# Kernel optimization log

Measured on AMD Instinct MI355X. Metric: run time of the kernel, lower is better.

The kernel has to match this reference:

```python
import jax, jax.numpy as jnp
import numpy as np

N_NODES = 50000
N_EDGES = 800000
IN_CH = 16
OUT_CH = 16


def setup_inputs() -> dict:
    key = jax.random.key(0)
    ks = jax.random.split(key, 12)
    s = lambda d: 1.0 / np.sqrt(d)
    return {
        "x": jax.random.normal(ks[0], (N_NODES, IN_CH), jnp.float32),
        "edge_index": jax.random.randint(ks[1], (2, N_EDGES), 0, N_NODES, jnp.int64),
        "edge_attr": jax.random.uniform(ks[2], (N_EDGES, 8), jnp.float32),
        "W1": jax.random.normal(ks[3], (8, 100), jnp.float32) * s(8),
        "b1": jnp.zeros((100,), jnp.float32),
        "W2": jax.random.normal(ks[4], (100, 100), jnp.float32) * s(100),
        "b2": jnp.zeros((100,), jnp.float32),
        "W3": jax.random.normal(ks[5], (100, 100), jnp.float32) * s(100),
        "b3": jnp.zeros((100,), jnp.float32),
        "W4": jax.random.normal(ks[6], (100, IN_CH * OUT_CH), jnp.float32) * s(100),
        "b4": jnp.zeros((IN_CH * OUT_CH,), jnp.float32),
        "root": jax.random.normal(ks[7], (IN_CH, OUT_CH), jnp.float32) * s(IN_CH),
        "bias": jnp.zeros((OUT_CH,), jnp.float32),
    }


def reference(x, edge_index, edge_attr, W1, b1, W2, b2, W3, b3, W4, b4, root, bias):
    src, dst = edge_index[0], edge_index[1]
    # edge MLP -> per-edge weight matrix [E, in, out]
    h = jax.nn.relu(edge_attr @ W1 + b1)
    h = jax.nn.relu(h @ W2 + b2)
    h = jax.nn.relu(h @ W3 + b3)
    w = (h @ W4 + b4).reshape(-1, IN_CH, OUT_CH)
    # gather source features, per-edge matmul
    msg = jnp.einsum('ei,eio->eo', x[src], w)  # [E, out]
    # scatter-mean into destination nodes
    agg = jax.ops.segment_sum(msg, dst, num_segments=N_NODES)
    cnt = jax.ops.segment_sum(jnp.ones((msg.shape[0],), msg.dtype), dst, num_segments=N_NODES)
    agg = agg / jnp.maximum(cnt, 1.0)[:, None]
    return x @ root + agg + bias
```

## Files before the change

kernel.cpp:

```cpp
#include <hip/hip_runtime.h>
#include <hip/hip_bf16.h>

constexpr int N_NODES = 50000;
constexpr int E_TOTAL = 800000;
constexpr int EB   = 32;
constexpr int NT   = E_TOTAL / EB;
constexpr int GRID = 768;
constexpr int TPB  = 256;

typedef __attribute__((ext_vector_type(8)))  short bf16x8;
typedef __attribute__((ext_vector_type(16))) float f32x16;

constexpr size_t WS_CNT = 0;
constexpr size_t WS_W1  = 200704;
constexpr size_t WS_W2  = WS_W1 + 4096;
constexpr size_t WS_W3  = WS_W2 + 32768;
constexpr size_t WS_W4  = WS_W3 + 32768;

constexpr int L_HA  = 0;
constexpr int L_HB  = 8704;
constexpr int L_EA  = 17408;
constexpr int L_XS  = 18944;
constexpr int L_MSG = 21504;
constexpr int L_DST = 31744;
constexpr int L_TOT = 32000;

__device__ inline unsigned short bfb(float f) {
    __hip_bfloat16 h = __float2bfloat16(f);
    return __builtin_bit_cast(unsigned short, h);
}
__device__ inline unsigned pk2(float a, float b) {
    return (unsigned)bfb(a) | ((unsigned)bfb(b) << 16);
}
__device__ inline unsigned pk2r(float a, float b) {
    return pk2(fmaxf(a, 0.f), fmaxf(b, 0.f));
}

template<int IN_OFF, int OUT_OFF>
__device__ inline void layer32(char* sm, const bf16x8 (&wf)[8],
                               int wn, int l31, int g)
{
    const int e = l31;
    f32x16 acc = {};
#pragma unroll
    for (int ks = 0; ks < 8; ++ks) {
        const bf16x8 b = *reinterpret_cast<const bf16x8*>(sm + IN_OFF + e * 272 + ks * 32 + g * 16);
        acc = __builtin_amdgcn_mfma_f32_32x32x16_bf16(wf[ks], b, acc, 0, 0, 0);
    }
#pragma unroll
    for (int q = 0; q < 4; ++q) {
        uint2 pk;
        pk.x = pk2r(acc[4 * q + 0], acc[4 * q + 1]);
        pk.y = pk2r(acc[4 * q + 2], acc[4 * q + 3]);
        *reinterpret_cast<uint2*>(sm + OUT_OFF + e * 272 + 64 * wn + 16 * q + 8 * g) = pk;
    }
}

__global__ __launch_bounds__(TPB, 3)
void edge_kernel(const float* __restrict__ x, const int* __restrict__ eidx,
                 const float* __restrict__ ea, const char* __restrict__ ws,
                 float* __restrict__ out, float* __restrict__ cnt)
{
    extern __shared__ char sm[];
    const int t    = threadIdx.x;
    const int lane = t & 63;
    const int wn   = t >> 6;
    const int l31  = lane & 31, g = lane >> 5;
    int* dsti = reinterpret_cast<int*>(sm + L_DST);

    bf16x8 wf1, wf2[8], wf3[8], wf4[2][8];
    {
        const int n = 32 * wn + l31;
        wf1 = *reinterpret_cast<const bf16x8*>(ws + WS_W1 + n * 32 + g * 16);
#pragma unroll
        for (int ks = 0; ks < 8; ++ks) {
            wf2[ks] = *reinterpret_cast<const bf16x8*>(ws + WS_W2 + n * 256 + ks * 32 + g * 16);
            wf3[ks] = *reinterpret_cast<const bf16x8*>(ws + WS_W3 + n * 256 + ks * 32 + g * 16);
        }
#pragma unroll
        for (int mf = 0; mf < 2; ++mf) {
            const int n4 = 64 * wn + 32 * mf + l31;
#pragma unroll
            for (int ks = 0; ks < 8; ++ks)
                wf4[mf][ks] = *reinterpret_cast<const bf16x8*>(ws + WS_W4 + n4 * 256 + ks * 32 + g * 16);
        }
    }

    if (t < 32)
        *reinterpret_cast<uint4*>(sm + L_EA + t * 48 + 16) = make_uint4(0x3F80u, 0u, 0u, 0u);

    float4 eaR, xvR; int dstR = 0;
    {
        const int e0 = blockIdx.x * EB;
        if (t < 64) eaR = *reinterpret_cast<const float4*>(&ea[(size_t)(e0 + (t >> 1)) * 8 + (t & 1) * 4]);
        if (t < 128) {
            const int s = eidx[e0 + (t >> 2)];
            xvR = *reinterpret_cast<const float4*>(&x[(size_t)s * 16 + (t & 3) * 4]);
        }
        if (t < 32) dstR = eidx[E_TOTAL + e0 + t];
    }

    int p = 0;
    bool has_prev = false;
    for (int tile = blockIdx.x; tile < NT; tile += GRID) {
        if (has_prev && t < 128) {
            const int e = t >> 2, o0 = (t & 3) * 4;
            const float4 s0 = *reinterpret_cast<const float4*>(sm + L_MSG + 0 * 2560 + e * 80 + o0 * 4);
            const float4 s1 = *reinterpret_cast<const float4*>(sm + L_MSG + 1 * 2560 + e * 80 + o0 * 4);
            const float4 s2 = *reinterpret_cast<const float4*>(sm + L_MSG + 2 * 2560 + e * 80 + o0 * 4);
            const float4 s3 = *reinterpret_cast<const float4*>(sm + L_MSG + 3 * 2560 + e * 80 + o0 * 4);
            const int d = dsti[(p ^ 1) * 32 + e];
            unsafeAtomicAdd(&out[(size_t)d * 16 + o0 + 0], s0.x + s1.x + s2.x + s3.x);
            unsafeAtomicAdd(&out[(size_t)d * 16 + o0 + 1], s0.y + s1.y + s2.y + s3.y);
            unsafeAtomicAdd(&out[(size_t)d * 16 + o0 + 2], s0.z + s1.z + s2.z + s3.z);
            unsafeAtomicAdd(&out[(size_t)d * 16 + o0 + 3], s0.w + s1.w + s2.w + s3.w);
            if ((t & 3) == 0) unsafeAtomicAdd(&cnt[d], 1.0f);
        }
        if (t < 64) {
            uint2 pk; pk.x = pk2(eaR.x, eaR.y); pk.y = pk2(eaR.z, eaR.w);
            *reinterpret_cast<uint2*>(sm + L_EA + (t >> 1) * 48 + 8 * (t & 1)) = pk;
        }
        if (t < 128)
            *reinterpret_cast<float4*>(sm + L_XS + (t >> 2) * 80 + (t & 3) * 16) = xvR;
        if (t < 32) dsti[p * 32 + t] = dstR;

        const int nxt = tile + GRID;
        if (nxt < NT) {
            const int e0 = nxt * EB;
            if (t < 64) eaR = *reinterpret_cast<const float4*>(&ea[(size_t)(e0 + (t >> 1)) * 8 + (t & 1) * 4]);
            if (t < 128) {
                const int s = eidx[e0 + (t >> 2)];
                xvR = *reinterpret_cast<const float4*>(&x[(size_t)s * 16 + (t & 3) * 4]);
            }
            if (t < 32) dstR = eidx[E_TOTAL + e0 + t];
        }
        __syncthreads();

        {
            const int e = l31;
            const bf16x8 b = *reinterpret_cast<const bf16x8*>(sm + L_EA + e * 48 + g * 16);
            f32x16 acc = {};
            acc = __builtin_amdgcn_mfma_f32_32x32x16_bf16(wf1, b, acc, 0, 0, 0);
#pragma unroll
            for (int q = 0; q < 4; ++q) {
                uint2 pk;
                pk.x = pk2r(acc[4 * q + 0], acc[4 * q + 1]);
                pk.y = pk2r(acc[4 * q + 2], acc[4 * q + 3]);
                *reinterpret_cast<uint2*>(sm + L_HA + e * 272 + 64 * wn + 16 * q + 8 * g) = pk;
            }
        }
        __syncthreads();
        layer32<L_HA, L_HB>(sm, wf2, wn, l31, g);
        __syncthreads();
        layer32<L_HB, L_HA>(sm, wf3, wn, l31, g);
        __syncthreads();

        {
            const int e = l31;
            f32x16 acc4[2] = {};
#pragma unroll
            for (int ks = 0; ks < 8; ++ks) {
                const bf16x8 b = *reinterpret_cast<const bf16x8*>(sm + L_HA + e * 272 + ks * 32 + g * 16);
#pragma unroll
                for (int mf = 0; mf < 2; ++mf)
                    acc4[mf] = __builtin_amdgcn_mfma_f32_32x32x16_bf16(wf4[mf][ks], b, acc4[mf], 0, 0, 0);
            }
            const float4 xv = *reinterpret_cast<const float4*>(sm + L_XS + e * 80 + wn * 16);
            float pr[8] = {0.f, 0.f, 0.f, 0.f, 0.f, 0.f, 0.f, 0.f};
#pragma unroll
            for (int mf = 0; mf < 2; ++mf)
#pragma unroll
                for (int reg = 0; reg < 16; ++reg) {
                    const float xi = (&xv.x)[2 * mf + (reg >> 3)];
                    const int s = (reg & 3) + 4 * ((reg >> 2) & 1);
                    pr[s] = fmaf(xi, acc4[mf][reg], pr[s]);
                }
            *reinterpret_cast<float4*>(sm + L_MSG + wn * 2560 + e * 80 + 16 * g) =
                make_float4(pr[0], pr[1], pr[2], pr[3]);
            *reinterpret_cast<float4*>(sm + L_MSG + wn * 2560 + e * 80 + 32 + 16 * g) =
                make_float4(pr[4], pr[5], pr[6], pr[7]);
        }
        __syncthreads();
        p ^= 1;
        has_prev = true;
    }

    if (has_prev && t < 128) {
        const int e = t >> 2, o0 = (t & 3) * 4;
        const float4 s0 = *reinterpret_cast<const float4*>(sm + L_MSG + 0 * 2560 + e * 80 + o0 * 4);
        const float4 s1 = *reinterpret_cast<const float4*>(sm + L_MSG + 1 * 2560 + e * 80 + o0 * 4);
        const float4 s2 = *reinterpret_cast<const float4*>(sm + L_MSG + 2 * 2560 + e * 80 + o0 * 4);
        const float4 s3 = *reinterpret_cast<const float4*>(sm + L_MSG + 3 * 2560 + e * 80 + o0 * 4);
        const int d = dsti[(p ^ 1) * 32 + e];
        unsafeAtomicAdd(&out[(size_t)d * 16 + o0 + 0], s0.x + s1.x + s2.x + s3.x);
        unsafeAtomicAdd(&out[(size_t)d * 16 + o0 + 1], s0.y + s1.y + s2.y + s3.y);
        unsafeAtomicAdd(&out[(size_t)d * 16 + o0 + 2], s0.z + s1.z + s2.z + s3.z);
        unsafeAtomicAdd(&out[(size_t)d * 16 + o0 + 3], s0.w + s1.w + s2.w + s3.w);
        if ((t & 3) == 0) unsafeAtomicAdd(&cnt[d], 1.0f);
    }
}

__global__ __launch_bounds__(256)
void prep_kernel(const float* __restrict__ W1, const float* __restrict__ b1,
                 const float* __restrict__ W2, const float* __restrict__ b2,
                 const float* __restrict__ W3, const float* __restrict__ b3,
                 const float* __restrict__ W4, const float* __restrict__ b4,
                 char* __restrict__ ws)
{
    const int id = blockIdx.x * 256 + threadIdx.x;
    if (id < N_NODES) reinterpret_cast<float*>(ws + WS_CNT)[id] = 0.f;
    if (id >= 67584) return;
    if (id < 2048) {
        const int n = id >> 4, k = id & 15;
        float v = 0.f;
        if (k < 8)        { if (n < 100) v = W1[k * 100 + n]; }
        else if (k == 8)  { v = (n < 100) ? b1[n] : (n == 100 ? 1.f : 0.f); }
        reinterpret_cast<unsigned short*>(ws + WS_W1)[id] = bfb(v);
    } else if (id < 18432) {
        const int j = id - 2048, n = j >> 7, k = j & 127;
        float v = 0.f;
        if (k < 100)       { if (n < 100) v = W2[k * 100 + n]; }
        else if (k == 100) { v = (n < 100) ? b2[n] : (n == 100 ? 1.f : 0.f); }
        reinterpret_cast<unsigned short*>(ws + WS_W2)[j] = bfb(v);
    } else if (id < 34816) {
        const int j = id - 18432, n = j >> 7, k = j & 127;
        float v = 0.f;
        if (k < 100)       { if (n < 100) v = W3[k * 100 + n]; }
        else if (k == 100) { v = (n < 100) ? b3[n] : (n == 100 ? 1.f : 0.f); }
        reinterpret_cast<unsigned short*>(ws + WS_W3)[j] = bfb(v);
    } else {
        const int j = id - 34816, n = j >> 7, k = j & 127;
        float v = 0.f;
        if (k < 100)       v = W4[k * 256 + n];
        else if (k == 100) v = b4[n];
        reinterpret_cast<unsigned short*>(ws + WS_W4)[j] = bfb(v);
    }
}

__global__ __launch_bounds__(256)
void node_kernel(const float* __restrict__ x, const float* __restrict__ root,
                 const float* __restrict__ bias, const float* __restrict__ cnt,
                 float* __restrict__ out)
{
    const int n = blockIdx.x * blockDim.x + threadIdx.x;
    if (n >= N_NODES) return;
    float xr[16];
#pragma unroll
    for (int q = 0; q < 4; ++q) {
        const float4 v = *reinterpret_cast<const float4*>(&x[(size_t)n * 16 + 4 * q]);
        xr[4 * q] = v.x; xr[4 * q + 1] = v.y; xr[4 * q + 2] = v.z; xr[4 * q + 3] = v.w;
    }
    const float inv = 1.f / fmaxf(cnt[n], 1.f);
#pragma unroll
    for (int q = 0; q < 4; ++q) {
        float4 o4 = *reinterpret_cast<float4*>(&out[(size_t)n * 16 + 4 * q]);
        float res[4];
#pragma unroll
        for (int j = 0; j < 4; ++j) {
            const int o = 4 * q + j;
            float dot = 0.f;
#pragma unroll
            for (int i = 0; i < 16; ++i)
                dot = fmaf(xr[i], root[i * 16 + o], dot);
            res[j] = dot + (&o4.x)[j] * inv + bias[o];
        }
        *reinterpret_cast<float4*>(&out[(size_t)n * 16 + 4 * q]) = make_float4(res[0], res[1], res[2], res[3]);
    }
}

extern "C" void kernel_launch(void* const* d_in, const int* in_sizes, int n_in,
                              void* d_out, int out_size, void* d_ws, size_t ws_size,
                              hipStream_t stream)
{
    const float* x    = (const float*)d_in[0];
    const int*   eidx = (const int*)  d_in[1];
    const float* ea   = (const float*)d_in[2];
    const float* W1   = (const float*)d_in[3];
    const float* b1   = (const float*)d_in[4];
    const float* W2   = (const float*)d_in[5];
    const float* b2   = (const float*)d_in[6];
    const float* W3   = (const float*)d_in[7];
    const float* b3   = (const float*)d_in[8];
    const float* W4   = (const float*)d_in[9];
    const float* b4   = (const float*)d_in[10];
    const float* root = (const float*)d_in[11];
    const float* bias = (const float*)d_in[12];
    float* out = (float*)d_out;
    char*  ws  = (char*)d_ws;
    float* cnt = (float*)d_ws;

    (void)in_sizes; (void)n_in; (void)ws_size;

    hipFuncSetAttribute((const void*)edge_kernel,
                        hipFuncAttributeMaxDynamicSharedMemorySize, L_TOT);

    hipMemsetAsync(d_out, 0, (size_t)out_size * sizeof(float), stream);

    hipLaunchKernelGGL(prep_kernel, dim3(264), dim3(256), 0, stream,
                       W1, b1, W2, b2, W3, b3, W4, b4, ws);
    hipLaunchKernelGGL(edge_kernel, dim3(GRID), dim3(TPB), L_TOT, stream,
                       x, eidx, ea, ws, out, cnt);
    hipLaunchKernelGGL(node_kernel, dim3((N_NODES + 255) / 256), dim3(256), 0, stream,
                       x, root, bias, cnt, out);
}
```

Before: 344.3 us.

## Software-pipeline edge MLP layers across tiles to halve barriers per tile

Restructures the per-tile loop into a two-stage software pipeline: layers 1-2 of the current tile run alongside layers 3-4 of the previous tile, with double/triple-buffered LDS for edge attrs, hidden activations, x rows, messages and dst indices. This cuts the barriers per tile from five to two and gives the scheduler independent MFMA work to interleave. The LDS footprint roughly doubles, so occupancy drops to 2 blocks per CU and the grid shrinks to 512. The extra bookkeeping and the lower occupancy may offset the gains from fewer barriers.

```diff
diff --git a/kernel.cpp b/kernel.cpp
--- a/kernel.cpp
+++ b/kernel.cpp
@@ -5,7 +5,7 @@
 constexpr int E_TOTAL = 800000;
 constexpr int EB   = 32;
 constexpr int NT   = E_TOTAL / EB;
-constexpr int GRID = 768;
+constexpr int GRID = 512;
 constexpr int TPB  = 256;
 
 typedef __attribute__((ext_vector_type(8)))  short bf16x8;
@@ -19,11 +19,12 @@
 
 constexpr int L_HA  = 0;
 constexpr int L_HB  = 8704;
-constexpr int L_EA  = 17408;
-constexpr int L_XS  = 18944;
-constexpr int L_MSG = 21504;
-constexpr int L_DST = 31744;
-constexpr int L_TOT = 32000;
+constexpr int L_HC  = 26112;
+constexpr int L_EA  = 34816;
+constexpr int L_XS  = 37888;
+constexpr int L_MSG = 45568;
+constexpr int L_DST = 66048;
+constexpr int L_TOT = 66560;
 
 __device__ inline unsigned short bfb(float f) {
     __hip_bfloat16 h = __float2bfloat16(f);
@@ -36,15 +37,14 @@
     return pk2(fmaxf(a, 0.f), fmaxf(b, 0.f));
 }
 
-template<int IN_OFF, int OUT_OFF>
 __device__ inline void layer32(char* sm, const bf16x8 (&wf)[8],
-                               int wn, int l31, int g)
+                               int inOff, int outOff, int wn, int l31, int g)
 {
     const int e = l31;
     f32x16 acc = {};
 #pragma unroll
     for (int ks = 0; ks < 8; ++ks) {
-        const bf16x8 b = *reinterpret_cast<const bf16x8*>(sm + IN_OFF + e * 272 + ks * 32 + g * 16);
+        const bf16x8 b = *reinterpret_cast<const bf16x8*>(sm + inOff + e * 272 + ks * 32 + g * 16);
         acc = __builtin_amdgcn_mfma_f32_32x32x16_bf16(wf[ks], b, acc, 0, 0, 0);
     }
 #pragma unroll
@@ -52,11 +52,11 @@
         uint2 pk;
         pk.x = pk2r(acc[4 * q + 0], acc[4 * q + 1]);
         pk.y = pk2r(acc[4 * q + 2], acc[4 * q + 3]);
-        *reinterpret_cast<uint2*>(sm + OUT_OFF + e * 272 + 64 * wn + 16 * q + 8 * g) = pk;
-    }
-}
-
-__global__ __launch_bounds__(TPB, 3)
+        *reinterpret_cast<uint2*>(sm + outOff + e * 272 + 64 * wn + 16 * q + 8 * g) = pk;
+    }
+}
+
+__global__ __launch_bounds__(TPB, 2)
 void edge_kernel(const float* __restrict__ x, const int* __restrict__ eidx,
                  const float* __restrict__ ea, const char* __restrict__ ws,
                  float* __restrict__ out, float* __restrict__ cnt)
@@ -66,7 +66,7 @@
     const int lane = t & 63;
     const int wn   = t >> 6;
     const int l31  = lane & 31, g = lane >> 5;
-    int* dsti = reinterpret_cast<int*>(sm + L_DST);
+    const int bid  = blockIdx.x;
 
     bf16x8 wf1, wf2[8], wf3[8], wf4[2][8];
     {
@@ -86,59 +86,74 @@
         }
     }
 
-    if (t < 32)
-        *reinterpret_cast<uint4*>(sm + L_EA + t * 48 + 16) = make_uint4(0x3F80u, 0u, 0u, 0u);
+    if (t < 64)
+        *reinterpret_cast<uint4*>(sm + L_EA + (t >> 5) * 1536 + (t & 31) * 48 + 16) =
+            make_uint4(0x3F80u, 0u, 0u, 0u);
+    {
+        const long e0 = (long)bid * EB;
+        if (t < 64) {
+            const float4 v = *reinterpret_cast<const float4*>(&ea[(e0 + (t >> 1)) * 8 + (t & 1) * 4]);
+            uint2 pk; pk.x = pk2(v.x, v.y); pk.y = pk2(v.z, v.w);
+            *reinterpret_cast<uint2*>(sm + L_EA + (t >> 1) * 48 + 8 * (t & 1)) = pk;
+        }
+        if (t < 128) {
+            const int s0 = eidx[e0 + (t >> 2)];
+            *reinterpret_cast<float4*>(sm + L_XS + (t >> 2) * 80 + (t & 3) * 16) =
+                *reinterpret_cast<const float4*>(&x[(size_t)s0 * 16 + (t & 3) * 4]);
+        }
+        if (t < 32)
+            reinterpret_cast<int*>(sm + L_DST)[t] = eidx[E_TOTAL + e0 + t];
+    }
+    __syncthreads();
 
     float4 eaR, xvR; int dstR = 0;
-    {
-        const int e0 = blockIdx.x * EB;
-        if (t < 64) eaR = *reinterpret_cast<const float4*>(&ea[(size_t)(e0 + (t >> 1)) * 8 + (t & 1) * 4]);
-        if (t < 128) {
-            const int s = eidx[e0 + (t >> 2)];
-            xvR = *reinterpret_cast<const float4*>(&x[(size_t)s * 16 + (t & 3) * 4]);
-        }
-        if (t < 32) dstR = eidx[E_TOTAL + e0 + t];
-    }
-
-    int p = 0;
-    bool has_prev = false;
-    for (int tile = blockIdx.x; tile < NT; tile += GRID) {
-        if (has_prev && t < 128) {
+
+    for (int s = 0; ; ++s) {
+        const long i = (long)bid + (long)s * GRID;
+        const bool vi  = i < NT;
+        const bool vm1 = (s >= 1) && (i - GRID) < NT;
+        const bool vm2 = (s >= 2) && (i - 2L * GRID) < NT;
+        if (!vi && !vm1 && !vm2) break;
+        const long ip1 = i + GRID;
+        const bool vp1 = ip1 < NT;
+
+        const int eaC  = s & 1;
+        const int eaN  = eaC ^ 1;
+        const int hbW  = s & 1;
+        const int hbR  = hbW ^ 1;
+        const int msW  = (s & 1) ^ 1;
+        const int msS  = s & 1;
+        const int xsR  = (s + 2) % 3;
+        const int xsW  = (s + 1) % 3;
+        const int dsS  = (s + 2) & 3;
+        const int dsW  = (s + 1) & 3;
+
+        if (vp1) {
+            const long e0 = ip1 * EB;
+            if (t < 64) eaR = *reinterpret_cast<const float4*>(&ea[(e0 + (t >> 1)) * 8 + (t & 1) * 4]);
+            if (t < 128) {
+                const int s0 = eidx[e0 + (t >> 2)];
+                xvR = *reinterpret_cast<const float4*>(&x[(size_t)s0 * 16 + (t & 3) * 4]);
+            }
+            if (t < 32) dstR = eidx[E_TOTAL + e0 + t];
+        }
+        if (vm2 && t < 128) {
             const int e = t >> 2, o0 = (t & 3) * 4;
-            const float4 s0 = *reinterpret_cast<const float4*>(sm + L_MSG + 0 * 2560 + e * 80 + o0 * 4);
-            const float4 s1 = *reinterpret_cast<const float4*>(sm + L_MSG + 1 * 2560 + e * 80 + o0 * 4);
-            const float4 s2 = *reinterpret_cast<const float4*>(sm + L_MSG + 2 * 2560 + e * 80 + o0 * 4);
-            const float4 s3 = *reinterpret_cast<const float4*>(sm + L_MSG + 3 * 2560 + e * 80 + o0 * 4);
-            const int d = dsti[(p ^ 1) * 32 + e];
+            const char* mb = sm + L_MSG + msS * 10240;
+            const float4 s0 = *reinterpret_cast<const float4*>(mb + 0 * 2560 + e * 80 + o0 * 4);
+            const float4 s1 = *reinterpret_cast<const float4*>(mb + 1 * 2560 + e * 80 + o0 * 4);
+            const float4 s2 = *reinterpret_cast<const float4*>(mb + 2 * 2560 + e * 80 + o0 * 4);
+            const float4 s3 = *reinterpret_cast<const float4*>(mb + 3 * 2560 + e * 80 + o0 * 4);
+            const int d = reinterpret_cast<const int*>(sm + L_DST)[dsS * 32 + e];
             unsafeAtomicAdd(&out[(size_t)d * 16 + o0 + 0], s0.x + s1.x + s2.x + s3.x);
             unsafeAtomicAdd(&out[(size_t)d * 16 + o0 + 1], s0.y + s1.y + s2.y + s3.y);
             unsafeAtomicAdd(&out[(size_t)d * 16 + o0 + 2], s0.z + s1.z + s2.z + s3.z);
             unsafeAtomicAdd(&out[(size_t)d * 16 + o0 + 3], s0.w + s1.w + s2.w + s3.w);
             if ((t & 3) == 0) unsafeAtomicAdd(&cnt[d], 1.0f);
         }
-        if (t < 64) {
-            uint2 pk; pk.x = pk2(eaR.x, eaR.y); pk.y = pk2(eaR.z, eaR.w);
-            *reinterpret_cast<uint2*>(sm + L_EA + (t >> 1) * 48 + 8 * (t & 1)) = pk;
-        }
-        if (t < 128)
-            *reinterpret_cast<float4*>(sm + L_XS + (t >> 2) * 80 + (t & 3) * 16) = xvR;
-        if (t < 32) dsti[p * 32 + t] = dstR;
-
-        const int nxt = tile + GRID;
-        if (nxt < NT) {
-            const int e0 = nxt * EB;
-            if (t < 64) eaR = *reinterpret_cast<const float4*>(&ea[(size_t)(e0 + (t >> 1)) * 8 + (t & 1) * 4]);
-            if (t < 128) {
-                const int s = eidx[e0 + (t >> 2)];
-                xvR = *reinterpret_cast<const float4*>(&x[(size_t)s * 16 + (t & 3) * 4]);
-            }
-            if (t < 32) dstR = eidx[E_TOTAL + e0 + t];
-        }
-        __syncthreads();
-
-        {
+        if (vi) {
             const int e = l31;
-            const bf16x8 b = *reinterpret_cast<const bf16x8*>(sm + L_EA + e * 48 + g * 16);
+            const bf16x8 b = *reinterpret_cast<const bf16x8*>(sm + L_EA + eaC * 1536 + e * 48 + g * 16);
             f32x16 acc = {};
             acc = __builtin_amdgcn_mfma_f32_32x32x16_bf16(wf1, b, acc, 0, 0, 0);
 #pragma unroll
@@ -149,54 +164,47 @@
                 *reinterpret_cast<uint2*>(sm + L_HA + e * 272 + 64 * wn + 16 * q + 8 * g) = pk;
             }
         }
+        if (vm1)
+            layer32(sm, wf3, L_HB + hbR * 8704, L_HC, wn, l31, g);
         __syncthreads();
-        layer32<L_HA, L_HB>(sm, wf2, wn, l31, g);
-        __syncthreads();
-        layer32<L_HB, L_HA>(sm, wf3, wn, l31, g);
-        __syncthreads();
-
-        {
+
+        if (vp1) {
+            if (t < 64) {
+                uint2 pk; pk.x = pk2(eaR.x, eaR.y); pk.y = pk2(eaR.z, eaR.w);
+                *reinterpret_cast<uint2*>(sm + L_EA + eaN * 1536 + (t >> 1) * 48 + 8 * (t & 1)) = pk;
+            }
+            if (t < 128)
+                *reinterpret_cast<float4*>(sm + L_XS + xsW * 2560 + (t >> 2) * 80 + (t & 3) * 16) = xvR;
+            if (t < 32)
+                reinterpret_cast<int*>(sm + L_DST)[dsW * 32 + t] = dstR;
+        }
+        if (vi)
+            layer32(sm, wf2, L_HA, L_HB + hbW * 8704, wn, l31, g);
+        if (vm1) {
             const int e = l31;
             f32x16 acc4[2] = {};
 #pragma unroll
             for (int ks = 0; ks < 8; ++ks) {
-                const bf16x8 b = *reinterpret_cast<const bf16x8*>(sm + L_HA + e * 272 + ks * 32 + g * 16);
+                const bf16x8 b = *reinterpret_cast<const bf16x8*>(sm + L_HC + e * 272 + ks * 32 + g * 16);
 #pragma unroll
                 for (int mf = 0; mf < 2; ++mf)
                     acc4[mf] = __builtin_amdgcn_mfma_f32_32x32x16_bf16(wf4[mf][ks], b, acc4[mf], 0, 0, 0);
             }
-            const float4 xv = *reinterpret_cast<const float4*>(sm + L_XS + e * 80 + wn * 16);
+            const float4 xv = *reinterpret_cast<const float4*>(sm + L_XS + xsR * 2560 + e * 80 + wn * 16);
             float pr[8] = {0.f, 0.f, 0.f, 0.f, 0.f, 0.f, 0.f, 0.f};
 #pragma unroll
             for (int mf = 0; mf < 2; ++mf)
 #pragma unroll
                 for (int reg = 0; reg < 16; ++reg) {
                     const float xi = (&xv.x)[2 * mf + (reg >> 3)];
-                    const int s = (reg & 3) + 4 * ((reg >> 2) & 1);
-                    pr[s] = fmaf(xi, acc4[mf][reg], pr[s]);
+                    const int sl = (reg & 3) + 4 * ((reg >> 2) & 1);
+                    pr[sl] = fmaf(xi, acc4[mf][reg], pr[sl]);
                 }
-            *reinterpret_cast<float4*>(sm + L_MSG + wn * 2560 + e * 80 + 16 * g) =
-                make_float4(pr[0], pr[1], pr[2], pr[3]);
-            *reinterpret_cast<float4*>(sm + L_MSG + wn * 2560 + e * 80 + 32 + 16 * g) =
-                make_float4(pr[4], pr[5], pr[6], pr[7]);
+            char* mb = sm + L_MSG + msW * 10240 + wn * 2560 + e * 80;
+            *reinterpret_cast<float4*>(mb + 16 * g)      = make_float4(pr[0], pr[1], pr[2], pr[3]);
+            *reinterpret_cast<float4*>(mb + 32 + 16 * g) = make_float4(pr[4], pr[5], pr[6], pr[7]);
         }
         __syncthreads();
-        p ^= 1;
-        has_prev = true;
-    }
-
-    if (has_prev && t < 128) {
-        const int e = t >> 2, o0 = (t & 3) * 4;
-        const float4 s0 = *reinterpret_cast<const float4*>(sm + L_MSG + 0 * 2560 + e * 80 + o0 * 4);
-        const float4 s1 = *reinterpret_cast<const float4*>(sm + L_MSG + 1 * 2560 + e * 80 + o0 * 4);
-        const float4 s2 = *reinterpret_cast<const float4*>(sm + L_MSG + 2 * 2560 + e * 80 + o0 * 4);
-        const float4 s3 = *reinterpret_cast<const float4*>(sm + L_MSG + 3 * 2560 + e * 80 + o0 * 4);
-        const int d = dsti[(p ^ 1) * 32 + e];
-        unsafeAtomicAdd(&out[(size_t)d * 16 + o0 + 0], s0.x + s1.x + s2.x + s3.x);
-        unsafeAtomicAdd(&out[(size_t)d * 16 + o0 + 1], s0.y + s1.y + s2.y + s3.y);
-        unsafeAtomicAdd(&out[(size_t)d * 16 + o0 + 2], s0.z + s1.z + s2.z + s3.z);
-        unsafeAtomicAdd(&out[(size_t)d * 16 + o0 + 3], s0.w + s1.w + s2.w + s3.w);
-        if ((t & 3) == 0) unsafeAtomicAdd(&cnt[d], 1.0f);
     }
 }
 
```

Measured after the change: 317.7 us. -7.7%, faster.
